# Performance work log

Measured on AMD Instinct MI355X. Metric: run time of the kernel, lower is better.

## Reference

```python
import jax, jax.numpy as jnp
import numpy as np

N = 100_000      # num nodes
E = 1_600_000    # num edges
IN = 128         # in_channels
H = 256          # hidden_channels
BN_EPS = 1e-5
L2_EPS = 1e-12


def setup_inputs() -> dict:
    key = jax.random.key(0)
    ks = jax.random.split(key, 12)
    x = jax.random.normal(ks[0], (N, IN), dtype=jnp.float32)
    edge_index = jax.random.randint(ks[1], (2, E), 0, N, dtype=jnp.int64)
    edge_weight = jax.random.uniform(ks[2], (E,), dtype=jnp.float32)
    s_in = 1.0 / np.sqrt(IN)
    s_h = 1.0 / np.sqrt(H)
    return {
        "x": x,
        "edge_index": edge_index,
        "edge_weight": edge_weight,
        # lin0 (skip projection)
        "W0": jax.random.normal(ks[3], (H, IN), jnp.float32) * s_in,
        "b0": jnp.zeros((H,), jnp.float32),
        # conv1
        "W1": jax.random.normal(ks[4], (H, IN), jnp.float32) * s_in,
        "b1": jnp.zeros((H,), jnp.float32),
        "g1": jnp.ones((H,), jnp.float32),
        "be1": jnp.zeros((H,), jnp.float32),
        "m1": jax.random.normal(ks[5], (H,), jnp.float32) * 0.1,
        "v1": jax.random.uniform(ks[6], (H,), jnp.float32, 0.5, 1.5),
        # conv2
        "W2": jax.random.normal(ks[7], (H, H), jnp.float32) * s_h,
        "b2": jnp.zeros((H,), jnp.float32),
        "g2": jnp.ones((H,), jnp.float32),
        "be2": jnp.zeros((H,), jnp.float32),
        "m2": jax.random.normal(ks[8], (H,), jnp.float32) * 0.1,
        "v2": jax.random.uniform(ks[9], (H,), jnp.float32, 0.5, 1.5),
        # classifier
        "Wc": jax.random.normal(ks[10], (2, H), jnp.float32) * s_h,
        "bc": jnp.zeros((2,), jnp.float32),
    }


def _gcn_conv(x, src, dst, ew, W, b):
    """PyG GCNConv: D^-1/2 (A + I) D^-1/2 X W^T + b (self-loop weight 1)."""
    h = x @ W.T                                            # [N, out]
    deg = jax.ops.segment_sum(ew, dst, num_segments=N) + 1.0  # weighted in-degree incl. self-loop
    dinv = jnp.where(deg > 0, jax.lax.rsqrt(deg), 0.0)     # [N]
    norm = dinv[src] * ew * dinv[dst]                      # [E]
    agg = jax.ops.segment_sum(norm[:, None] * h[src], dst, num_segments=N)
    agg = agg + (dinv * dinv)[:, None] * h                 # self-loop term
    return agg + b


def _bn_eval(x, g, beta, m, v):
    return (x - m) * jax.lax.rsqrt(v + BN_EPS) * g + beta


def _l2norm(x):
    n = jnp.sqrt(jnp.sum(x * x, axis=1, keepdims=True))
    return x / jnp.maximum(n, L2_EPS)


def reference(x, edge_index, edge_weight, W0, b0, W1, b1, g1, be1, m1, v1,
              W2, b2, g2, be2, m2, v2, Wc, bc):
    src, dst = edge_index[0], edge_index[1]
    x0 = x @ W0.T + b0                                     # lin0 skip
    x1 = _gcn_conv(x, src, dst, edge_weight, W1, b1)
    x1 = jax.nn.relu(_bn_eval(x1, g1, be1, m1, v1))        # dropout = identity (eval)
    x1 = _l2norm(x1) + 0.2 * x0
    x2 = _gcn_conv(x1, src, dst, edge_weight, W2, b2)
    x2 = _bn_eval(x2, g2, be2, m2, v2)
    x2 = _l2norm(x2)
    embeddings = x2 + 0.5 * x1
    logits = embeddings @ Wc.T + bc
    return embeddings, logits
```

## Files before the change

kernel.cpp:

```cpp
#include <hip/hip_runtime.h>

#define NN 100000
#define EE 1600000
#define NBIN 196
#define CAPB 8704

typedef short bf16x8 __attribute__((ext_vector_type(8)));
typedef float f32x4 __attribute__((ext_vector_type(4)));

__device__ __forceinline__ float bl(unsigned int u) { return __uint_as_float(u << 16); }
__device__ __forceinline__ float bh(unsigned int u) { return __uint_as_float(u & 0xffff0000u); }
__device__ __forceinline__ unsigned short f2b(float f) {
  unsigned int u = __float_as_uint(f);
  return (unsigned short)((u + 0x7fffu + ((u >> 16) & 1u)) >> 16);
}
__device__ __forceinline__ float wsum(float v) {
#pragma unroll
  for (int o = 32; o; o >>= 1) v += __shfl_xor(v, o);
  return v;
}
__device__ __forceinline__ void g2l16(const void* g, void* l) {
  __builtin_amdgcn_global_load_lds((const __attribute__((address_space(1))) unsigned int*)g,
                                   (__attribute__((address_space(3))) unsigned int*)l, 16, 0, 0);
}

__global__ void k_zero(int* cnt, int n) {
  int i = blockIdx.x * 256 + threadIdx.x;
  if (i < n) cnt[i] = 0;
}

__global__ __launch_bounds__(256) void k_build(
    const int* __restrict__ src, const int* __restrict__ dst,
    const float* __restrict__ ew, int* gcnt, uint2* __restrict__ gbuf,
    const float* __restrict__ x, unsigned short* __restrict__ xb,
    const float* __restrict__ W1, const float* __restrict__ W0,
    const float* __restrict__ W2, unsigned short* __restrict__ Wcat,
    unsigned short* __restrict__ W2b)
{
  const int b = blockIdx.x;
  if (b < 391) {
    __shared__ uint2 est[4096];
    __shared__ int lhist[NBIN], lbase[NBIN], lcur[NBIN];
    const int tid = threadIdx.x;
    for (int t = tid; t < NBIN; t += 256) { lhist[t] = 0; lcur[t] = 0; }
    __syncthreads();
    const int e0 = b * 4096;
    const int ne = min(4096, EE - e0);
    for (int k = tid; k < ne; k += 256) {
      int e = e0 + k;
      int d = dst[e];
      int bin = d >> 9, low = d & 511;
      int q = min(__float2int_rn(ew[e] * 32768.0f), 32767);
      est[k] = make_uint2((unsigned)src[e],
                          ((unsigned)bin << 24) | ((unsigned)q << 9) | (unsigned)low);
      atomicAdd(&lhist[bin], 1);
    }
    __syncthreads();
    for (int t = tid; t < NBIN; t += 256)
      lbase[t] = lhist[t] ? atomicAdd(&gcnt[t], lhist[t]) : 0;
    __syncthreads();
    for (int k = tid; k < ne; k += 256) {
      uint2 E = est[k];
      int bin = E.y >> 24;
      int p = lbase[bin] + atomicAdd(&lcur[bin], 1);
      if (p < CAPB) gbuf[(size_t)bin * CAPB + p] = make_uint2(E.x, E.y & 0x00FFFFFFu);
    }
  } else if (b < 12891) {
    int i = (b - 391) * 256 + threadIdx.x;
    float4 v = ((const float4*)x)[i];
    uint2 o;
    o.x = (unsigned int)f2b(v.x) | ((unsigned int)f2b(v.y) << 16);
    o.y = (unsigned int)f2b(v.z) | ((unsigned int)f2b(v.w) << 16);
    ((uint2*)xb)[i] = o;
  } else {
    int wb = b - 12891;
    const float* in;
    unsigned short* out;
    int idx;
    if (wb < 32)      { in = W1; out = Wcat;             idx = wb * 256 + threadIdx.x; }
    else if (wb < 64) { in = W0; out = Wcat + 256 * 128; idx = (wb - 32) * 256 + threadIdx.x; }
    else              { in = W2; out = W2b;              idx = (wb - 64) * 256 + threadIdx.x; }
    float4 v = ((const float4*)in)[idx];
    uint2 o;
    o.x = (unsigned int)f2b(v.x) | ((unsigned int)f2b(v.y) << 16);
    o.y = (unsigned int)f2b(v.z) | ((unsigned int)f2b(v.w) << 16);
    ((uint2*)out)[idx] = o;
  }
}

__global__ __launch_bounds__(256) void k_phase2(
    const uint2* __restrict__ gbuf, const int* __restrict__ gcnt,
    unsigned int* __restrict__ csr, int2* __restrict__ ntab, float* __restrict__ dinv)
{
  __shared__ uint2 ebuf[CAPB];
  __shared__ unsigned int obuf[CAPB];
  __shared__ int hist[512];
  __shared__ float wsm[512];
  __shared__ int cur[512];
  __shared__ int psum[256];
  const int g = blockIdx.x, tid = threadIdx.x;
  for (int t = tid; t < 512; t += 256) { hist[t] = 0; wsm[t] = 0.f; }
  __syncthreads();
  const int cn = min(gcnt[g], CAPB);
  for (int j = tid; j < cn; j += 256) {
    uint2 E = gbuf[(size_t)g * CAPB + j];
    ebuf[j] = E;
    int low = E.y & 511;
    atomicAdd(&hist[low], 1);
    atomicAdd(&wsm[low], (float)(E.y >> 9) * (1.0f / 32768.0f));
  }
  __syncthreads();
  int h0 = hist[2 * tid], h1 = hist[2 * tid + 1];
  int pair = h0 + h1;
  psum[tid] = pair;
  __syncthreads();
  for (int off = 1; off < 256; off <<= 1) {
    int v = (tid >= off) ? psum[tid - off] : 0;
    __syncthreads();
    psum[tid] += v;
    __syncthreads();
  }
  int exb = psum[tid] - pair;
  int ex0 = exb, ex1 = exb + h0;
  cur[2 * tid] = ex0;
  cur[2 * tid + 1] = ex1;
  int n0 = g * 512 + 2 * tid;
  if (n0 < NN) {
    ntab[n0] = make_int2(g * CAPB + ex0, h0);
    dinv[n0] = rsqrtf(wsm[2 * tid] + 1.0f);
  }
  if (n0 + 1 < NN) {
    ntab[n0 + 1] = make_int2(g * CAPB + ex1, h1);
    dinv[n0 + 1] = rsqrtf(wsm[2 * tid + 1] + 1.0f);
  }
  __syncthreads();
  for (int j = tid; j < cn; j += 256) {
    uint2 E = ebuf[j];
    int low = E.y & 511;
    int p = atomicAdd(&cur[low], 1);
    obuf[p] = E.x | ((E.y >> 9) << 17);
  }
  __syncthreads();
  for (int j = tid; j < cn; j += 256) csr[(size_t)g * CAPB + j] = obuf[j];
}

template <int COLS>
__global__ __launch_bounds__(256) void k_aggregate(
    const unsigned short* __restrict__ h, const int2* __restrict__ ntab,
    const unsigned int* __restrict__ csr, const float* __restrict__ dinv,
    unsigned short* __restrict__ out)
{
  __shared__ int2 sm[4][64];
  const int wid = threadIdx.x >> 6, lane = threadIdx.x & 63;
  const int i = blockIdx.x * 4 + wid;
  constexpr int VPL = COLS / 64;
  const int2 nt = ntab[i];
  const int beg = nt.x, cn = nt.y;
  float acc[VPL];
#pragma unroll
  for (int k = 0; k < VPL; ++k) acc[k] = 0.f;
  for (int base = 0; base < cn; base += 64) {
    const int chunk = min(64, cn - base);
    int2 ent;
    if (lane < chunk) {
      unsigned int u = csr[beg + base + lane];
      int s = (int)(u & 0x1FFFFu);
      float nr = (float)(u >> 17) * (1.0f / 32768.0f) * dinv[s];
      ent = make_int2(s, __float_as_int(nr));
    } else {
      ent = make_int2(i, 0);
    }
    sm[wid][lane] = ent;
    for (int sub = 0; sub < chunk; sub += 8) {
      int2 e[8];
#pragma unroll
      for (int k = 0; k < 8; ++k) e[k] = sm[wid][sub + k];
      if constexpr (VPL == 4) {
        uint2 u[8];
#pragma unroll
        for (int k = 0; k < 8; ++k)
          u[k] = *(const uint2*)(h + (size_t)e[k].x * COLS + lane * 4);
#pragma unroll
        for (int k = 0; k < 8; ++k) {
          float nr = __int_as_float(e[k].y);
          acc[0] = fmaf(nr, bl(u[k].x), acc[0]);
          acc[1] = fmaf(nr, bh(u[k].x), acc[1]);
          acc[2] = fmaf(nr, bl(u[k].y), acc[2]);
          acc[3] = fmaf(nr, bh(u[k].y), acc[3]);
        }
      } else {
        unsigned int u[8];
#pragma unroll
        for (int k = 0; k < 8; ++k)
          u[k] = *(const unsigned int*)(h + (size_t)e[k].x * COLS + lane * 2);
#pragma unroll
        for (int k = 0; k < 8; ++k) {
          float nr = __int_as_float(e[k].y);
          acc[0] = fmaf(nr, bl(u[k]), acc[0]);
          acc[1] = fmaf(nr, bh(u[k]), acc[1]);
        }
      }
    }
  }
  const float di = dinv[i];
  const unsigned short* op = h + (size_t)i * COLS + lane * VPL;
  if constexpr (VPL == 4) {
    uint2 u = *(const uint2*)op;
    float r0 = di * (acc[0] + di * bl(u.x));
    float r1 = di * (acc[1] + di * bh(u.x));
    float r2 = di * (acc[2] + di * bl(u.y));
    float r3 = di * (acc[3] + di * bh(u.y));
    uint2 o;
    o.x = (unsigned int)f2b(r0) | ((unsigned int)f2b(r1) << 16);
    o.y = (unsigned int)f2b(r2) | ((unsigned int)f2b(r3) << 16);
    *(uint2*)(out + (size_t)i * COLS + lane * VPL) = o;
  } else {
    unsigned int u = *(const unsigned int*)op;
    float r0 = di * (acc[0] + di * bl(u));
    float r1 = di * (acc[1] + di * bh(u));
    unsigned int o = (unsigned int)f2b(r0) | ((unsigned int)f2b(r1) << 16);
    *(unsigned int*)(out + (size_t)i * COLS + lane * VPL) = o;
  }
}

__global__ __launch_bounds__(256) void k_mgemm(
    const unsigned short* __restrict__ A0, const unsigned short* __restrict__ A1, int nsplit,
    const unsigned short* __restrict__ B, unsigned short* __restrict__ C,
    int M, int K, int ldc)
{
  __shared__ __align__(16) unsigned short Als[128 * 64];
  __shared__ __align__(16) unsigned short Bls[128 * 64];
  const int tid = threadIdx.x;
  const int w = tid >> 6, l = tid & 63;
  const int m0 = blockIdx.x * 128, n0 = blockIdx.y * 128;
  const unsigned short* __restrict__ A = (n0 < nsplit) ? A0 : A1;
  const int wr = w >> 1, wc = w & 1;
  const int lr = l >> 3;
  const int lc = l & 7;
  const int fr = l & 15;
  const int fk = l >> 4;
  f32x4 acc[4][4];
#pragma unroll
  for (int m = 0; m < 4; ++m)
#pragma unroll
    for (int n = 0; n < 4; ++n)
#pragma unroll
      for (int q = 0; q < 4; ++q) acc[m][n][q] = 0.f;

  for (int k0 = 0; k0 < K; k0 += 64) {
#pragma unroll
    for (int i2 = 0; i2 < 4; ++i2) {
      const int ob = (w * 4 + i2) * 1024;
      const int r = (ob >> 7) + lr;
      const int c = lc ^ (r & 7);
      int rg = m0 + r; if (rg >= M) rg = M - 1;
      g2l16(A + (size_t)rg * K + k0 + c * 8, (char*)Als + ob);
      g2l16(B + (size_t)(n0 + r) * K + k0 + c * 8, (char*)Bls + ob);
    }
    __syncthreads();
#pragma unroll
    for (int ks = 0; ks < 2; ++ks) {
      bf16x8 af[4], bfr[4];
#pragma unroll
      for (int m = 0; m < 4; ++m) {
        const int r = wr * 64 + m * 16 + fr;
        const int cc = (ks * 4 + fk) ^ (r & 7);
        af[m] = *(const bf16x8*)((const char*)Als + r * 128 + cc * 16);
      }
#pragma unroll
      for (int n = 0; n < 4; ++n) {
        const int r = wc * 64 + n * 16 + fr;
        const int cc = (ks * 4 + fk) ^ (r & 7);
        bfr[n] = *(const bf16x8*)((const char*)Bls + r * 128 + cc * 16);
      }
#pragma unroll
      for (int m = 0; m < 4; ++m)
#pragma unroll
        for (int n = 0; n < 4; ++n)
          acc[m][n] = __builtin_amdgcn_mfma_f32_16x16x32_bf16(af[m], bfr[n], acc[m][n], 0, 0, 0);
    }
    __syncthreads();
  }
#pragma unroll
  for (int m = 0; m < 4; ++m) {
    const int rbase = m0 + wr * 64 + m * 16 + fk * 4;
#pragma unroll
    for (int n = 0; n < 4; ++n) {
      const int col = n0 + wc * 64 + n * 16 + fr;
#pragma unroll
      for (int q = 0; q < 4; ++q) {
        const int row = rbase + q;
        if (row < M) C[(size_t)row * ldc + col] = f2b(acc[m][n][q]);
      }
    }
  }
}

__global__ __launch_bounds__(256) void k_post1(
    const unsigned short* __restrict__ C1, const float* __restrict__ b1,
    const float* __restrict__ g1, const float* __restrict__ be1,
    const float* __restrict__ m1, const float* __restrict__ v1,
    const float* __restrict__ b0, unsigned short* __restrict__ x1b)
{
  const int wid = threadIdx.x >> 6, lane = threadIdx.x & 63;
  const int i = blockIdx.x * 4 + wid;
  const int c0 = lane * 4;
  uint2 uh = *(const uint2*)(C1 + (size_t)i * 512 + c0);
  uint2 ux = *(const uint2*)(C1 + (size_t)i * 512 + 256 + c0);
  float hv[4] = {bl(uh.x), bh(uh.x), bl(uh.y), bh(uh.y)};
  float x0[4] = {bl(ux.x), bh(ux.x), bl(ux.y), bh(ux.y)};
  float ss = 0.f;
#pragma unroll
  for (int j = 0; j < 4; ++j) {
    const int c = c0 + j;
    float t = hv[j] + b1[c];
    t = (t - m1[c]) * rsqrtf(v1[c] + 1e-5f) * g1[c] + be1[c];
    t = fmaxf(t, 0.f);
    hv[j] = t;
    ss += t * t;
  }
  ss = wsum(ss);
  const float rn = 1.f / fmaxf(sqrtf(ss), 1e-12f);
  float r[4];
#pragma unroll
  for (int j = 0; j < 4; ++j) r[j] = fmaf(hv[j], rn, 0.2f * (x0[j] + b0[c0 + j]));
  uint2 o;
  o.x = (unsigned int)f2b(r[0]) | ((unsigned int)f2b(r[1]) << 16);
  o.y = (unsigned int)f2b(r[2]) | ((unsigned int)f2b(r[3]) << 16);
  *(uint2*)(x1b + (size_t)i * 256 + c0) = o;
}

__global__ __launch_bounds__(256) void k_aggpost2(
    const unsigned short* __restrict__ t, const unsigned short* __restrict__ x1b,
    const int2* __restrict__ ntab, const unsigned int* __restrict__ csr,
    const float* __restrict__ dinv,
    const float* __restrict__ b2, const float* __restrict__ g2,
    const float* __restrict__ be2, const float* __restrict__ m2,
    const float* __restrict__ v2, const float* __restrict__ Wc,
    const float* __restrict__ bc, float* __restrict__ outE, float* __restrict__ outL)
{
  __shared__ int2 sm[4][64];
  const int wid = threadIdx.x >> 6, lane = threadIdx.x & 63;
  const int i = blockIdx.x * 4 + wid;
  const int c0 = lane * 4;
  const int2 nt = ntab[i];
  const int beg = nt.x, cn = nt.y;
  float acc[4] = {0.f, 0.f, 0.f, 0.f};
  for (int base = 0; base < cn; base += 64) {
    const int chunk = min(64, cn - base);
    int2 ent;
    if (lane < chunk) {
      unsigned int u = csr[beg + base + lane];
      int s = (int)(u & 0x1FFFFu);
      float nr = (float)(u >> 17) * (1.0f / 32768.0f) * dinv[s];
      ent = make_int2(s, __float_as_int(nr));
    } else {
      ent = make_int2(i, 0);
    }
    sm[wid][lane] = ent;
    for (int sub = 0; sub < chunk; sub += 8) {
      int2 e[8];
#pragma unroll
      for (int k = 0; k < 8; ++k) e[k] = sm[wid][sub + k];
      uint2 u[8];
#pragma unroll
      for (int k = 0; k < 8; ++k)
        u[k] = *(const uint2*)(t + (size_t)e[k].x * 256 + c0);
#pragma unroll
      for (int k = 0; k < 8; ++k) {
        float nr = __int_as_float(e[k].y);
        acc[0] = fmaf(nr, bl(u[k].x), acc[0]);
        acc[1] = fmaf(nr, bh(u[k].x), acc[1]);
        acc[2] = fmaf(nr, bl(u[k].y), acc[2]);
        acc[3] = fmaf(nr, bh(u[k].y), acc[3]);
      }
    }
  }
  const float di = dinv[i];
  uint2 us = *(const uint2*)(t + (size_t)i * 256 + c0);
  float self[4] = {bl(us.x), bh(us.x), bl(us.y), bh(us.y)};
  uint2 uk = *(const uint2*)(x1b + (size_t)i * 256 + c0);
  float sk[4] = {bl(uk.x), bh(uk.x), bl(uk.y), bh(uk.y)};
  float ss = 0.f;
  float hv[4];
#pragma unroll
  for (int j = 0; j < 4; ++j) {
    const int c = c0 + j;
    float r = di * (acc[j] + di * self[j]) + b2[c];
    r = (r - m2[c]) * rsqrtf(v2[c] + 1e-5f) * g2[c] + be2[c];
    hv[j] = r;
    ss += r * r;
  }
  ss = wsum(ss);
  const float rn = 1.f / fmaxf(sqrtf(ss), 1e-12f);
  float e4[4];
  float s0 = 0.f, s1 = 0.f;
#pragma unroll
  for (int j = 0; j < 4; ++j) {
    e4[j] = fmaf(hv[j], rn, 0.5f * sk[j]);
    s0 = fmaf(e4[j], Wc[c0 + j], s0);
    s1 = fmaf(e4[j], Wc[256 + c0 + j], s1);
  }
  *(float4*)(outE + (size_t)i * 256 + c0) = make_float4(e4[0], e4[1], e4[2], e4[3]);
  s0 = wsum(s0);
  s1 = wsum(s1);
  if (lane == 0) {
    outL[(size_t)i * 2] = s0 + bc[0];
    outL[(size_t)i * 2 + 1] = s1 + bc[1];
  }
}

extern "C" void kernel_launch(void* const* d_in, const int* in_sizes, int n_in,
                              void* d_out, int out_size, void* d_ws, size_t ws_size,
                              hipStream_t stream) {
  const float* x   = (const float*)d_in[0];
  const int*   ei  = (const int*)d_in[1];
  const float* ew  = (const float*)d_in[2];
  const float* W0  = (const float*)d_in[3];
  const float* b0  = (const float*)d_in[4];
  const float* W1  = (const float*)d_in[5];
  const float* b1  = (const float*)d_in[6];
  const float* g1  = (const float*)d_in[7];
  const float* be1 = (const float*)d_in[8];
  const float* m1  = (const float*)d_in[9];
  const float* v1  = (const float*)d_in[10];
  const float* W2  = (const float*)d_in[11];
  const float* b2  = (const float*)d_in[12];
  const float* g2  = (const float*)d_in[13];
  const float* be2 = (const float*)d_in[14];
  const float* m2  = (const float*)d_in[15];
  const float* v2  = (const float*)d_in[16];
  const float* Wc  = (const float*)d_in[17];
  const float* bc  = (const float*)d_in[18];
  const int* srcp = ei;
  const int* dstp = ei + EE;

  char* w = (char*)d_ws;
  auto alloc = [&](size_t bytes) {
    char* p = w;
    w += (bytes + 255) & ~(size_t)255;
    return p;
  };
  unsigned short* xb     = (unsigned short*)alloc((size_t)NN * 128 * 2);
  unsigned short* ax     = (unsigned short*)alloc((size_t)NN * 128 * 2);
  unsigned short* x1b    = (unsigned short*)alloc((size_t)NN * 256 * 2);
  unsigned short* C1     = (unsigned short*)alloc((size_t)NN * 512 * 2);
  unsigned short* t2     = C1;
  unsigned short* Wcat   = (unsigned short*)alloc((size_t)512 * 128 * 2);
  unsigned short* W2b    = (unsigned short*)alloc((size_t)256 * 256 * 2);
  float*          dinvv  = (float*)alloc((size_t)NN * 4);
  int*            gcnt   = (int*)alloc((size_t)NBIN * 4);
  uint2*          gbuf   = (uint2*)alloc((size_t)NBIN * CAPB * 8);
  unsigned int*   csr    = (unsigned int*)alloc((size_t)NBIN * CAPB * 4);
  int2*           ntab   = (int2*)alloc((size_t)NN * 8);

  float* outEmb = (float*)d_out;
  float* outLog = outEmb + (size_t)NN * 256;

  const int NW = NN / 4;

  k_zero<<<1, 256, 0, stream>>>(gcnt, NBIN);
  k_build<<<13019, 256, 0, stream>>>(srcp, dstp, ew, gcnt, gbuf,
                                     x, xb, W1, W0, W2, Wcat, W2b);
  k_phase2<<<NBIN, 256, 0, stream>>>(gbuf, gcnt, csr, ntab, dinvv);

  k_aggregate<128><<<NW, 256, 0, stream>>>(xb, ntab, csr, dinvv, ax);
  dim3 g1d((NN + 127) / 128, 4);
  k_mgemm<<<g1d, 256, 0, stream>>>(ax, xb, 256, Wcat, C1, NN, 128, 512);
  k_post1<<<NW, 256, 0, stream>>>(C1, b1, g1, be1, m1, v1, b0, x1b);

  dim3 g2d((NN + 127) / 128, 2);
  k_mgemm<<<g2d, 256, 0, stream>>>(x1b, x1b, 1 << 28, W2b, t2, NN, 256, 256);
  k_aggpost2<<<NW, 256, 0, stream>>>(t2, x1b, ntab, csr, dinvv,
                                     b2, g2, be2, m2, v2, Wc, bc, outEmb, outLog);
}
```

Measured before the change: 365.8 us.

## Co-schedule skip GEMM with layer-1 aggregation and fuse post1 into GEMM epilogue

The layer-1 aggregation kernel now interleaves, in every 17th block, a tile of the x@W0 skip-projection GEMM, so the compute-bound GEMM overlaps the memory-bound gather. A new GEMM kernel computes the full 256-column conv1 output per 128-row tile and applies bias, batch-norm, ReLU, a row L2 norm reduced via shuffles and LDS, and the skip add in its epilogue, which removes the separate post1 pass and the 512-wide intermediate. This costs more registers per block (launch bounds of two blocks per CU), an extra x0 buffer round trip, and scattered 2-byte epilogue stores.

```diff
diff --git a/kernel.cpp b/kernel.cpp
--- a/kernel.cpp
+++ b/kernel.cpp
@@ -10,6 +10,7 @@
 
 __device__ __forceinline__ float bl(unsigned int u) { return __uint_as_float(u << 16); }
 __device__ __forceinline__ float bh(unsigned int u) { return __uint_as_float(u & 0xffff0000u); }
+__device__ __forceinline__ float b2f(unsigned short s) { return __uint_as_float((unsigned int)s << 16); }
 __device__ __forceinline__ unsigned short f2b(float f) {
   unsigned int u = __float_as_uint(f);
   return (unsigned short)((u + 0x7fffu + ((u >> 16) & 1u)) >> 16);
@@ -144,55 +145,104 @@
   for (int j = tid; j < cn; j += 256) csr[(size_t)g * CAPB + j] = obuf[j];
 }
 
-template <int COLS>
-__global__ __launch_bounds__(256) void k_aggregate(
-    const unsigned short* __restrict__ h, const int2* __restrict__ ntab,
+__global__ __launch_bounds__(256) void k_l1a(
+    const unsigned short* __restrict__ xb, const int2* __restrict__ ntab,
     const unsigned int* __restrict__ csr, const float* __restrict__ dinv,
-    unsigned short* __restrict__ out)
+    unsigned short* __restrict__ ax,
+    const unsigned short* __restrict__ Wcat, unsigned short* __restrict__ x0b)
 {
-  __shared__ int2 sm[4][64];
-  const int wid = threadIdx.x >> 6, lane = threadIdx.x & 63;
-  const int i = blockIdx.x * 4 + wid;
-  constexpr int VPL = COLS / 64;
-  const int2 nt = ntab[i];
-  const int beg = nt.x, cn = nt.y;
-  float acc[VPL];
-#pragma unroll
-  for (int k = 0; k < VPL; ++k) acc[k] = 0.f;
-  for (int base = 0; base < cn; base += 64) {
-    const int chunk = min(64, cn - base);
-    int2 ent;
-    if (lane < chunk) {
-      unsigned int u = csr[beg + base + lane];
-      int s = (int)(u & 0x1FFFFu);
-      float nr = (float)(u >> 17) * (1.0f / 32768.0f) * dinv[s];
-      ent = make_int2(s, __float_as_int(nr));
-    } else {
-      ent = make_int2(i, 0);
-    }
-    sm[wid][lane] = ent;
-    for (int sub = 0; sub < chunk; sub += 8) {
-      int2 e[8];
-#pragma unroll
-      for (int k = 0; k < 8; ++k) e[k] = sm[wid][sub + k];
-      if constexpr (VPL == 4) {
-        uint2 u[8];
+  __shared__ __align__(16) char lsmem[16384];
+  const int b = blockIdx.x;
+  const int q = b / 17, r17 = b % 17;
+  const int tid = threadIdx.x;
+  const int w = tid >> 6, l = tid & 63;
+
+  if (r17 == 16) {
+    unsigned short* Als = (unsigned short*)lsmem;
+    unsigned short* Bls = Als + 128 * 32;
+    const unsigned short* __restrict__ W0b = Wcat + 256 * 128;
+    const int m0 = (q >> 1) * 128, n0 = (q & 1) * 128;
+    const int wr = w >> 1, wc = w & 1;
+    const int lr = l >> 2, lc = l & 3, fr = l & 15, fk = l >> 4;
+    f32x4 acc[4][4];
+#pragma unroll
+    for (int m = 0; m < 4; ++m)
+#pragma unroll
+      for (int n = 0; n < 4; ++n)
+#pragma unroll
+        for (int qq = 0; qq < 4; ++qq) acc[m][n][qq] = 0.f;
+    for (int k0 = 0; k0 < 128; k0 += 32) {
+#pragma unroll
+      for (int i2 = 0; i2 < 2; ++i2) {
+        const int ob = (w * 2 + i2) * 1024;
+        const int r = (ob >> 6) + lr;
+        const int c = lc ^ (r & 3);
+        int rg = m0 + r; if (rg >= NN) rg = NN - 1;
+        g2l16(xb + (size_t)rg * 128 + k0 + c * 8, (char*)Als + ob);
+        g2l16(W0b + (size_t)(n0 + r) * 128 + k0 + c * 8, (char*)Bls + ob);
+      }
+      __syncthreads();
+      bf16x8 af[4], bfr[4];
+#pragma unroll
+      for (int m = 0; m < 4; ++m) {
+        const int rA = wr * 64 + m * 16 + fr;
+        const int cc = fk ^ (rA & 3);
+        af[m] = *(const bf16x8*)((const char*)Als + rA * 64 + cc * 16);
+      }
+#pragma unroll
+      for (int n = 0; n < 4; ++n) {
+        const int rB = wc * 64 + n * 16 + fr;
+        const int cc = fk ^ (rB & 3);
+        bfr[n] = *(const bf16x8*)((const char*)Bls + rB * 64 + cc * 16);
+      }
+#pragma unroll
+      for (int m = 0; m < 4; ++m)
+#pragma unroll
+        for (int n = 0; n < 4; ++n)
+          acc[m][n] = __builtin_amdgcn_mfma_f32_16x16x32_bf16(af[m], bfr[n], acc[m][n], 0, 0, 0);
+      __syncthreads();
+    }
+#pragma unroll
+    for (int m = 0; m < 4; ++m) {
+      const int rbase = m0 + wr * 64 + m * 16 + fk * 4;
+#pragma unroll
+      for (int n = 0; n < 4; ++n) {
+        const int col = n0 + wc * 64 + n * 16 + fr;
+#pragma unroll
+        for (int qq = 0; qq < 4; ++qq) {
+          const int row = rbase + qq;
+          if (row < NN) x0b[(size_t)row * 256 + col] = f2b(acc[m][n][qq]);
+        }
+      }
+    }
+  } else {
+    const int a = q * 16 + r17;
+    if (a >= 25000) return;
+    int2* sm = ((int2*)lsmem) + w * 64;
+    const int i = a * 4 + w;
+    const int2 nt = ntab[i];
+    const int beg = nt.x, cn = nt.y;
+    float acc[2] = {0.f, 0.f};
+    for (int base = 0; base < cn; base += 64) {
+      const int chunk = min(64, cn - base);
+      int2 ent;
+      if (l < chunk) {
+        unsigned int u = csr[beg + base + l];
+        int s = (int)(u & 0x1FFFFu);
+        float nr = (float)(u >> 17) * (1.0f / 32768.0f) * dinv[s];
+        ent = make_int2(s, __float_as_int(nr));
+      } else {
+        ent = make_int2(i, 0);
+      }
+      sm[l] = ent;
+      for (int sub = 0; sub < chunk; sub += 8) {
+        int2 e[8];
+#pragma unroll
+        for (int k = 0; k < 8; ++k) e[k] = sm[sub + k];
+        unsigned int u[8];
 #pragma unroll
         for (int k = 0; k < 8; ++k)
-          u[k] = *(const uint2*)(h + (size_t)e[k].x * COLS + lane * 4);
-#pragma unroll
-        for (int k = 0; k < 8; ++k) {
-          float nr = __int_as_float(e[k].y);
-          acc[0] = fmaf(nr, bl(u[k].x), acc[0]);
-          acc[1] = fmaf(nr, bh(u[k].x), acc[1]);
-          acc[2] = fmaf(nr, bl(u[k].y), acc[2]);
-          acc[3] = fmaf(nr, bh(u[k].y), acc[3]);
-        }
-      } else {
-        unsigned int u[8];
-#pragma unroll
-        for (int k = 0; k < 8; ++k)
-          u[k] = *(const unsigned int*)(h + (size_t)e[k].x * COLS + lane * 2);
+          u[k] = *(const unsigned int*)(xb + (size_t)e[k].x * 128 + l * 2);
 #pragma unroll
         for (int k = 0; k < 8; ++k) {
           float nr = __int_as_float(e[k].y);
@@ -201,26 +251,153 @@
         }
       }
     }
-  }
-  const float di = dinv[i];
-  const unsigned short* op = h + (size_t)i * COLS + lane * VPL;
-  if constexpr (VPL == 4) {
-    uint2 u = *(const uint2*)op;
-    float r0 = di * (acc[0] + di * bl(u.x));
-    float r1 = di * (acc[1] + di * bh(u.x));
-    float r2 = di * (acc[2] + di * bl(u.y));
-    float r3 = di * (acc[3] + di * bh(u.y));
-    uint2 o;
-    o.x = (unsigned int)f2b(r0) | ((unsigned int)f2b(r1) << 16);
-    o.y = (unsigned int)f2b(r2) | ((unsigned int)f2b(r3) << 16);
-    *(uint2*)(out + (size_t)i * COLS + lane * VPL) = o;
-  } else {
-    unsigned int u = *(const unsigned int*)op;
-    float r0 = di * (acc[0] + di * bl(u));
-    float r1 = di * (acc[1] + di * bh(u));
+    const float di = dinv[i];
+    unsigned int us = *(const unsigned int*)(xb + (size_t)i * 128 + l * 2);
+    float r0 = di * (acc[0] + di * bl(us));
+    float r1 = di * (acc[1] + di * bh(us));
     unsigned int o = (unsigned int)f2b(r0) | ((unsigned int)f2b(r1) << 16);
-    *(unsigned int*)(out + (size_t)i * COLS + lane * VPL) = o;
-  }
+    *(unsigned int*)(ax + (size_t)i * 128 + l * 2) = o;
+  }
+}
+
+__global__ __launch_bounds__(256, 2) void k_gemm1f(
+    const unsigned short* __restrict__ A, const unsigned short* __restrict__ Wcat,
+    const unsigned short* __restrict__ x0b,
+    const float* __restrict__ b0, const float* __restrict__ b1,
+    const float* __restrict__ g1, const float* __restrict__ be1,
+    const float* __restrict__ m1, const float* __restrict__ v1,
+    unsigned short* __restrict__ x1b)
+{
+  __shared__ __align__(16) unsigned short Als[128 * 64];
+  __shared__ __align__(16) unsigned short Bls[256 * 64];
+  __shared__ float rss[2][128];
+  const int tid = threadIdx.x;
+  const int w = tid >> 6, l = tid & 63;
+  const int m0 = blockIdx.x * 128;
+  const int wr = w >> 1, wcb = w & 1;
+  const int lr = l >> 3, lc = l & 7, fr = l & 15, fk = l >> 4;
+  f32x4 acc[2][4][4];
+#pragma unroll
+  for (int ct = 0; ct < 2; ++ct)
+#pragma unroll
+    for (int m = 0; m < 4; ++m)
+#pragma unroll
+      for (int n = 0; n < 4; ++n)
+#pragma unroll
+        for (int qq = 0; qq < 4; ++qq) acc[ct][m][n][qq] = 0.f;
+
+  for (int k0 = 0; k0 < 128; k0 += 64) {
+#pragma unroll
+    for (int i2 = 0; i2 < 4; ++i2) {
+      const int ob = (w * 4 + i2) * 1024;
+      const int r = (ob >> 7) + lr;
+      const int c = lc ^ (r & 7);
+      int rg = m0 + r; if (rg >= NN) rg = NN - 1;
+      g2l16(A + (size_t)rg * 128 + k0 + c * 8, (char*)Als + ob);
+    }
+#pragma unroll
+    for (int i2 = 0; i2 < 8; ++i2) {
+      const int ob = (w * 8 + i2) * 1024;
+      const int r = (ob >> 7) + lr;
+      const int c = lc ^ (r & 7);
+      g2l16(Wcat + (size_t)r * 128 + k0 + c * 8, (char*)Bls + ob);
+    }
+    __syncthreads();
+#pragma unroll
+    for (int ks = 0; ks < 2; ++ks) {
+      bf16x8 af[4], bfr[2][4];
+#pragma unroll
+      for (int m = 0; m < 4; ++m) {
+        const int rA = wr * 64 + m * 16 + fr;
+        const int cc = (ks * 4 + fk) ^ (rA & 7);
+        af[m] = *(const bf16x8*)((const char*)Als + rA * 128 + cc * 16);
+      }
+#pragma unroll
+      for (int ct = 0; ct < 2; ++ct)
+#pragma unroll
+        for (int n = 0; n < 4; ++n) {
+          const int rB = (wcb + 2 * ct) * 64 + n * 16 + fr;
+          const int cc = (ks * 4 + fk) ^ (rB & 7);
+          bfr[ct][n] = *(const bf16x8*)((const char*)Bls + rB * 128 + cc * 16);
+        }
+#pragma unroll
+      for (int ct = 0; ct < 2; ++ct)
+#pragma unroll
+        for (int m = 0; m < 4; ++m)
+#pragma unroll
+          for (int n = 0; n < 4; ++n)
+            acc[ct][m][n] = __builtin_amdgcn_mfma_f32_16x16x32_bf16(af[m], bfr[ct][n], acc[ct][m][n], 0, 0, 0);
+    }
+    __syncthreads();
+  }
+
+  float A2[2][4], B2[2][4], C2[2][4];
+#pragma unroll
+  for (int ct = 0; ct < 2; ++ct)
+#pragma unroll
+    for (int n = 0; n < 4; ++n) {
+      const int c = (wcb + 2 * ct) * 64 + n * 16 + fr;
+      float sc = g1[c] * rsqrtf(v1[c] + 1e-5f);
+      A2[ct][n] = sc;
+      B2[ct][n] = (b1[c] - m1[c]) * sc + be1[c];
+      C2[ct][n] = 0.2f * b0[c];
+    }
+  float ssp[4][4];
+#pragma unroll
+  for (int m = 0; m < 4; ++m)
+#pragma unroll
+    for (int qq = 0; qq < 4; ++qq) ssp[m][qq] = 0.f;
+#pragma unroll
+  for (int ct = 0; ct < 2; ++ct)
+#pragma unroll
+    for (int m = 0; m < 4; ++m)
+#pragma unroll
+      for (int n = 0; n < 4; ++n)
+#pragma unroll
+        for (int qq = 0; qq < 4; ++qq) {
+          float t = fmaxf(acc[ct][m][n][qq] * A2[ct][n] + B2[ct][n], 0.f);
+          acc[ct][m][n][qq] = t;
+          ssp[m][qq] += t * t;
+        }
+#pragma unroll
+  for (int o = 1; o < 16; o <<= 1)
+#pragma unroll
+    for (int m = 0; m < 4; ++m)
+#pragma unroll
+      for (int qq = 0; qq < 4; ++qq) ssp[m][qq] += __shfl_xor(ssp[m][qq], o);
+  if (fr == 0) {
+#pragma unroll
+    for (int m = 0; m < 4; ++m)
+#pragma unroll
+      for (int qq = 0; qq < 4; ++qq)
+        rss[wcb][wr * 64 + m * 16 + fk * 4 + qq] = ssp[m][qq];
+  }
+  __syncthreads();
+  float rn[4][4];
+#pragma unroll
+  for (int m = 0; m < 4; ++m)
+#pragma unroll
+    for (int qq = 0; qq < 4; ++qq) {
+      const int r128 = wr * 64 + m * 16 + fk * 4 + qq;
+      rn[m][qq] = 1.f / fmaxf(sqrtf(rss[0][r128] + rss[1][r128]), 1e-12f);
+    }
+#pragma unroll
+  for (int ct = 0; ct < 2; ++ct)
+#pragma unroll
+    for (int m = 0; m < 4; ++m)
+#pragma unroll
+      for (int n = 0; n < 4; ++n) {
+        const int col = (wcb + 2 * ct) * 64 + n * 16 + fr;
+#pragma unroll
+        for (int qq = 0; qq < 4; ++qq) {
+          const int row = m0 + wr * 64 + m * 16 + fk * 4 + qq;
+          if (row < NN) {
+            float x0v = b2f(x0b[(size_t)row * 256 + col]);
+            float rv = acc[ct][m][n][qq] * rn[m][qq] + 0.2f * x0v + C2[ct][n];
+            x1b[(size_t)row * 256 + col] = f2b(rv);
+          }
+        }
+      }
 }
 
 __global__ __launch_bounds__(256) void k_mgemm(
@@ -294,40 +471,6 @@
       }
     }
   }
-}
-
-__global__ __launch_bounds__(256) void k_post1(
-    const unsigned short* __restrict__ C1, const float* __restrict__ b1,
-    const float* __restrict__ g1, const float* __restrict__ be1,
-    const float* __restrict__ m1, const float* __restrict__ v1,
-    const float* __restrict__ b0, unsigned short* __restrict__ x1b)
-{
-  const int wid = threadIdx.x >> 6, lane = threadIdx.x & 63;
-  const int i = blockIdx.x * 4 + wid;
-  const int c0 = lane * 4;
-  uint2 uh = *(const uint2*)(C1 + (size_t)i * 512 + c0);
-  uint2 ux = *(const uint2*)(C1 + (size_t)i * 512 + 256 + c0);
-  float hv[4] = {bl(uh.x), bh(uh.x), bl(uh.y), bh(uh.y)};
-  float x0[4] = {bl(ux.x), bh(ux.x), bl(ux.y), bh(ux.y)};
-  float ss = 0.f;
-#pragma unroll
-  for (int j = 0; j < 4; ++j) {
-    const int c = c0 + j;
-    float t = hv[j] + b1[c];
-    t = (t - m1[c]) * rsqrtf(v1[c] + 1e-5f) * g1[c] + be1[c];
-    t = fmaxf(t, 0.f);
-    hv[j] = t;
-    ss += t * t;
-  }
-  ss = wsum(ss);
-  const float rn = 1.f / fmaxf(sqrtf(ss), 1e-12f);
-  float r[4];
-#pragma unroll
-  for (int j = 0; j < 4; ++j) r[j] = fmaf(hv[j], rn, 0.2f * (x0[j] + b0[c0 + j]));
-  uint2 o;
-  o.x = (unsigned int)f2b(r[0]) | ((unsigned int)f2b(r[1]) << 16);
-  o.y = (unsigned int)f2b(r[2]) | ((unsigned int)f2b(r[3]) << 16);
-  *(uint2*)(x1b + (size_t)i * 256 + c0) = o;
 }
 
 __global__ __launch_bounds__(256) void k_aggpost2(
@@ -443,9 +586,9 @@
   };
   unsigned short* xb     = (unsigned short*)alloc((size_t)NN * 128 * 2);
   unsigned short* ax     = (unsigned short*)alloc((size_t)NN * 128 * 2);
+  unsigned short* x0b    = (unsigned short*)alloc((size_t)NN * 256 * 2);
   unsigned short* x1b    = (unsigned short*)alloc((size_t)NN * 256 * 2);
-  unsigned short* C1     = (unsigned short*)alloc((size_t)NN * 512 * 2);
-  unsigned short* t2     = C1;
+  unsigned short* t2     = (unsigned short*)alloc((size_t)NN * 256 * 2);
   unsigned short* Wcat   = (unsigned short*)alloc((size_t)512 * 128 * 2);
   unsigned short* W2b    = (unsigned short*)alloc((size_t)256 * 256 * 2);
   float*          dinvv  = (float*)alloc((size_t)NN * 4);
@@ -457,20 +600,16 @@
   float* outEmb = (float*)d_out;
   float* outLog = outEmb + (size_t)NN * 256;
 
-  const int NW = NN / 4;
-
   k_zero<<<1, 256, 0, stream>>>(gcnt, NBIN);
   k_build<<<13019, 256, 0, stream>>>(srcp, dstp, ew, gcnt, gbuf,
                                      x, xb, W1, W0, W2, Wcat, W2b);
   k_phase2<<<NBIN, 256, 0, stream>>>(gbuf, gcnt, csr, ntab, dinvv);
 
-  k_aggregate<128><<<NW, 256, 0, stream>>>(xb, ntab, csr, dinvv, ax);
-  dim3 g1d((NN + 127) / 128, 4);
-  k_mgemm<<<g1d, 256, 0, stream>>>(ax, xb, 256, Wcat, C1, NN, 128, 512);
-  k_post1<<<NW, 256, 0, stream>>>(C1, b1, g1, be1, m1, v1, b0, x1b);
+  k_l1a<<<26588, 256, 0, stream>>>(xb, ntab, csr, dinvv, ax, Wcat, x0b);
+  k_gemm1f<<<782, 256, 0, stream>>>(ax, Wcat, x0b, b0, b1, g1, be1, m1, v1, x1b);
 
   dim3 g2d((NN + 127) / 128, 2);
   k_mgemm<<<g2d, 256, 0, stream>>>(x1b, x1b, 1 << 28, W2b, t2, NN, 256, 256);
-  k_aggpost2<<<NW, 256, 0, stream>>>(t2, x1b, ntab, csr, dinvv,
-                                     b2, g2, be2, m2, v2, Wc, bc, outEmb, outLog);
-}
+  k_aggpost2<<<25000, 256, 0, stream>>>(t2, x1b, ntab, csr, dinvv,
+                                        b2, g2, be2, m2, v2, Wc, bc, outEmb, outLog);
+}
```

Result: slower. 426.8 us (+16.7%).
